# Kernel tuning notes

Hardware: AMD Instinct MI355X
Metric: run time of the kernel (lower is better)

The kernel has to match this reference:

```python
import jax, jax.numpy as jnp
import numpy as np

B, N, HW, PS, FHW = 16, 4096, 224, 8, 56

def _gelu(x):
    return jax.nn.gelu(x, approximate=True)  # tanh approximation, matches nn.GELU(approximate='tanh')

def _conv(x, w, b, stride):
    y = jax.lax.conv_general_dilated(x, w, (stride, stride), [(1, 1), (1, 1)],
                                     dimension_numbers=('NCHW', 'OIHW', 'NCHW'))
    return y + b[None, :, None, None]

def _embed(points):
    # for i in 0..11: append sin(2^i * p) then cos(2^i * p) -> [B,N,48]
    factors = 2.0 ** jnp.arange(12, dtype=points.dtype)
    scaled = points[..., None, :] * factors[:, None]          # [B,N,12,2]
    feats = jnp.concatenate([jnp.sin(scaled), jnp.cos(scaled)], axis=-1)  # [B,N,12,4]
    return feats.reshape(points.shape[0], points.shape[1], 48)

def _extract_patches(fmap, points):
    # fmap [B,C,H,W]; points in [0,1]; bilinear grid_sample, zeros padding, align_corners=True
    Bq, C, H, W = fmap.shape
    centers = points * 2.0 - 1.0
    step = 2.0 / (W - 1)
    half = (PS - 1) / 2.0
    offs = jnp.linspace(-half, half, PS, dtype=fmap.dtype) * step
    offx2d, offy2d = jnp.meshgrid(offs, offs, indexing='ij')   # [ps,ps]
    gx = centers[..., 0][..., None, None] + offx2d             # [B,N,ps,ps]
    gy = centers[..., 1][..., None, None] + offy2d
    # align_corners=True pixel coords
    ix = (gx + 1.0) * 0.5 * (W - 1)
    iy = (gy + 1.0) * 0.5 * (H - 1)
    x0f = jnp.floor(ix); y0f = jnp.floor(iy)
    x0 = x0f.astype(jnp.int32); y0 = y0f.astype(jnp.int32)
    x1 = x0 + 1; y1 = y0 + 1
    wx1 = ix - x0f; wx0 = 1.0 - wx1
    wy1 = iy - y0f; wy0 = 1.0 - wy1
    fflat = fmap.reshape(Bq, C, H * W)

    def corner(xi, yi, w):
        valid = ((xi >= 0) & (xi < W) & (yi >= 0) & (yi < H)).astype(fmap.dtype)
        idx = jnp.clip(yi, 0, H - 1) * W + jnp.clip(xi, 0, W - 1)   # [B,N,ps,ps]
        vals = jax.vmap(lambda f, i: f[:, i])(fflat, idx)           # [B,C,N,ps,ps]
        return vals * (w * valid)[:, None]

    out = (corner(x0, y0, wx0 * wy0) + corner(x1, y0, wx1 * wy0)
           + corner(x0, y1, wx0 * wy1) + corner(x1, y1, wx1 * wy1))  # [B,C,N,ps,ps]
    return out.transpose(0, 2, 1, 3, 4)                              # [B,N,C,ps,ps]

def setup_inputs():
    key = jax.random.key(0)
    ks = jax.random.split(key, 26)
    def w(k, shape):
        fan_in = int(np.prod(shape[1:]))
        return jax.random.normal(k, shape, jnp.float32) * (1.0 / np.sqrt(fan_in))
    inp = {
        'points': jax.random.uniform(ks[0], (B, N, 2), jnp.float32),
        'images': jax.random.normal(ks[1], (B, 3, HW, HW), jnp.float32),
        # plane encoder
        'pw1': w(ks[2], (16, 3, 3, 3)),  'pb1': jnp.zeros((16,), jnp.float32),
        'pw2': w(ks[3], (32, 16, 3, 3)), 'pb2': jnp.zeros((32,), jnp.float32),
        'pw3': w(ks[4], (4, 32, 3, 3)),  'pb3': jnp.zeros((4,), jnp.float32),
        # global encoder
        'gw1': w(ks[5], (4, 3, 3, 3)),   'gb1': jnp.zeros((4,), jnp.float32),
        'gw2': w(ks[6], (8, 4, 3, 3)),   'gb2': jnp.zeros((8,), jnp.float32),
        'gw3': w(ks[7], (16, 8, 3, 3)),  'gb3': jnp.zeros((16,), jnp.float32),
        'gw4': w(ks[8], (32, 16, 3, 3)), 'gb4': jnp.zeros((32,), jnp.float32),
        'gw5': w(ks[9], (64, 32, 3, 3)), 'gb5': jnp.zeros((64,), jnp.float32),
        # point encoder (torch Linear: [out,in])
        'lw1': w(ks[10], (256, 48)),  'lb1': jnp.zeros((256,), jnp.float32),
        'lw2': w(ks[11], (256, 256)), 'lb2': jnp.zeros((256,), jnp.float32),
        # head
        'hw1': w(ks[12], (512, 576)), 'hb1': jnp.zeros((512,), jnp.float32),
        'hw2': w(ks[13], (1, 512)),   'hb2': jnp.zeros((1,), jnp.float32),
    }
    return inp

def reference(points, images, pw1, pb1, pw2, pb2, pw3, pb3,
              gw1, gb1, gw2, gb2, gw3, gb3, gw4, gb4, gw5, gb5,
              lw1, lb1, lw2, lb2, hw1, hb1, hw2, hb2):
    # point branch
    pe = _embed(points)                                         # [B,N,48]
    pf = _gelu(pe @ lw1.T + lb1) @ lw2.T + lb2                  # [B,N,256]
    # plane encoder -> 4x56x56 fmap
    f = _gelu(_conv(images, pw1, pb1, 2))
    f = _gelu(_conv(f, pw2, pb2, 2))
    fmap = _gelu(_conv(f, pw3, pb3, 1))                         # [B,4,56,56]
    # global encoder -> [B,64]
    g = images
    for wg, bg in ((gw1, gb1), (gw2, gb2), (gw3, gb3), (gw4, gb4), (gw5, gb5)):
        g = _gelu(_conv(g, wg, bg, 2))
    gc = g.mean(axis=(2, 3))                                    # AvgPool2d(7)+Flatten -> [B,64]
    gc = jnp.broadcast_to(gc[:, None, :], (points.shape[0], points.shape[1], 64))
    # per-point bilinear patch gather
    patches = _extract_patches(fmap, points).reshape(points.shape[0], points.shape[1], -1)  # [B,N,256]
    fused = jnp.concatenate([pf, patches, gc], axis=-1)         # [B,N,576]
    logit = _gelu(fused @ hw1.T + hb1) @ hw2.T + hb2            # [B,N,1]
    return logit
```

## Files before the change

kernel.cpp:

```cpp
#include <hip/hip_runtime.h>
#include <math.h>

#define BB 16
#define NN 4096
#define M_TOT (BB*NN)
#define TBK 32

typedef __attribute__((ext_vector_type(8))) short s8v;
typedef __attribute__((ext_vector_type(4))) float f4v;

__device__ __forceinline__ float gelu_t(float x){
    float u = 1.5957691216057308f * x * (1.0f + 0.044715f*x*x);
    return x / (1.0f + __expf(-u));
}

__device__ __forceinline__ unsigned short f2bf(float f){
    unsigned int u = __float_as_uint(f);
    u += 0x7fffu + ((u >> 16) & 1u);
    return (unsigned short)(u >> 16);
}

#define GLL(src, dst) __builtin_amdgcn_global_load_lds( \
    (const __attribute__((address_space(1))) void*)(src), \
    (__attribute__((address_space(3))) void*)(dst), 16, 0, 0)

template<int CIN, int COUT, int STRIDE>
__global__ __launch_bounds__(256) void conv_tile_k(
    const float* __restrict__ in, const float* __restrict__ w,
    const float* __restrict__ bias, float* __restrict__ out,
    int Hin, int Win, int Hout, int Wout)
{
    constexpr int IW = 15*STRIDE + 3;
    constexpr int IH = IW;
    __shared__ float tile[IH][IW + 1];
    int tid = threadIdx.x;
    int tx = tid & 15, ty = tid >> 4;
    int b = blockIdx.z;
    int wo = blockIdx.x*16 + tx;
    int ho = blockIdx.y*16 + ty;
    int win0 = blockIdx.x*16*STRIDE - 1;
    int hin0 = blockIdx.y*16*STRIDE - 1;
    bool valid = (wo < Wout) && (ho < Hout);

    float acc[COUT];
    #pragma unroll
    for (int co = 0; co < COUT; ++co) acc[co] = bias[co];

    const float* ib = in + (size_t)(b*CIN)*Hin*Win;
    for (int ci = 0; ci < CIN; ++ci) {
        __syncthreads();
        const float* ic = ib + (size_t)ci*Hin*Win;
        for (int idx = tid; idx < IH*IW; idx += 256) {
            int r = idx / IW, c = idx - r*IW;
            int hi = hin0 + r, wi = win0 + c;
            float v = 0.f;
            if ((unsigned)hi < (unsigned)Hin && (unsigned)wi < (unsigned)Win)
                v = ic[hi*Win + wi];
            tile[r][c] = v;
        }
        __syncthreads();
        float vv[9];
        #pragma unroll
        for (int kh = 0; kh < 3; ++kh)
            #pragma unroll
            for (int kw = 0; kw < 3; ++kw)
                vv[kh*3+kw] = tile[ty*STRIDE + kh][tx*STRIDE + kw];
        const float* wc = w + ci*9;
        #pragma unroll
        for (int co = 0; co < COUT; ++co) {
            const float* wp = wc + co*CIN*9;
            #pragma unroll
            for (int k = 0; k < 9; ++k)
                acc[co] = fmaf(vv[k], wp[k], acc[co]);
        }
    }
    if (valid) {
        size_t obase = ((size_t)b*COUT)*Hout*Wout + (size_t)ho*Wout + wo;
        #pragma unroll
        for (int co = 0; co < COUT; ++co)
            out[obase + (size_t)co*Hout*Wout] = gelu_t(acc[co]);
    }
}

__global__ __launch_bounds__(256) void conv_p3_k(
    const float* __restrict__ in, const float* __restrict__ w,
    const float* __restrict__ bias, float4* __restrict__ out)
{
    __shared__ float tile[18][19];
    int tid = threadIdx.x;
    int tx = tid & 15, ty = tid >> 4;
    int b = blockIdx.z;
    int wo = blockIdx.x*16 + tx;
    int ho = blockIdx.y*16 + ty;
    int win0 = blockIdx.x*16 - 1;
    int hin0 = blockIdx.y*16 - 1;
    bool valid = (ho < 56) && (wo < 56);

    float acc[4];
    #pragma unroll
    for (int co = 0; co < 4; ++co) acc[co] = bias[co];

    const float* ib = in + (size_t)(b*32)*3136;
    for (int ci = 0; ci < 32; ++ci) {
        __syncthreads();
        const float* ic = ib + (size_t)ci*3136;
        for (int idx = tid; idx < 18*18; idx += 256) {
            int r = idx / 18, c = idx - r*18;
            int hi = hin0 + r, wi = win0 + c;
            float v = 0.f;
            if ((unsigned)hi < 56u && (unsigned)wi < 56u)
                v = ic[hi*56 + wi];
            tile[r][c] = v;
        }
        __syncthreads();
        float vv[9];
        #pragma unroll
        for (int kh = 0; kh < 3; ++kh)
            #pragma unroll
            for (int kw = 0; kw < 3; ++kw)
                vv[kh*3+kw] = tile[ty + kh][tx + kw];
        #pragma unroll
        for (int co = 0; co < 4; ++co) {
            const float* wp = w + co*288 + ci*9;
            #pragma unroll
            for (int k = 0; k < 9; ++k)
                acc[co] = fmaf(vv[k], wp[k], acc[co]);
        }
    }
    if (valid) {
        float4 o;
        o.x = gelu_t(acc[0]); o.y = gelu_t(acc[1]);
        o.z = gelu_t(acc[2]); o.w = gelu_t(acc[3]);
        out[(size_t)b*3136 + (size_t)ho*56 + wo] = o;
    }
}

__global__ __launch_bounds__(256) void conv_dual_k(
    const float* __restrict__ in,
    const float* __restrict__ wA, const float* __restrict__ bA,
    const float* __restrict__ wB, const float* __restrict__ bB,
    float* __restrict__ outA, float* __restrict__ outB)
{
    constexpr int IW = 33, IH = 33;
    const int Hin = 224, Win = 224, Hout = 112, Wout = 112;
    __shared__ float tile[IH][IW + 1];
    int tid = threadIdx.x;
    int tx = tid & 15, ty = tid >> 4;
    int b = blockIdx.z;
    int wo = blockIdx.x*16 + tx;
    int ho = blockIdx.y*16 + ty;
    int win0 = blockIdx.x*32 - 1;
    int hin0 = blockIdx.y*32 - 1;

    float accA[16], accB[4];
    #pragma unroll
    for (int co = 0; co < 16; ++co) accA[co] = bA[co];
    #pragma unroll
    for (int co = 0; co < 4; ++co) accB[co] = bB[co];

    const float* ib = in + (size_t)(b*3)*Hin*Win;
    for (int ci = 0; ci < 3; ++ci) {
        __syncthreads();
        const float* ic = ib + (size_t)ci*Hin*Win;
        for (int idx = tid; idx < IH*IW; idx += 256) {
            int r = idx / IW, c = idx - r*IW;
            int hi = hin0 + r, wi = win0 + c;
            float v = 0.f;
            if ((unsigned)hi < (unsigned)Hin && (unsigned)wi < (unsigned)Win)
                v = ic[hi*Win + wi];
            tile[r][c] = v;
        }
        __syncthreads();
        float vv[9];
        #pragma unroll
        for (int kh = 0; kh < 3; ++kh)
            #pragma unroll
            for (int kw = 0; kw < 3; ++kw)
                vv[kh*3+kw] = tile[ty*2 + kh][tx*2 + kw];
        #pragma unroll
        for (int co = 0; co < 16; ++co) {
            const float* wp = wA + co*27 + ci*9;
            #pragma unroll
            for (int k = 0; k < 9; ++k) accA[co] = fmaf(vv[k], wp[k], accA[co]);
        }
        #pragma unroll
        for (int co = 0; co < 4; ++co) {
            const float* wp = wB + co*27 + ci*9;
            #pragma unroll
            for (int k = 0; k < 9; ++k) accB[co] = fmaf(vv[k], wp[k], accB[co]);
        }
    }
    size_t px = (size_t)ho*Wout + wo;
    #pragma unroll
    for (int co = 0; co < 16; ++co)
        outA[((size_t)(b*16 + co))*Hout*Wout + px] = gelu_t(accA[co]);
    #pragma unroll
    for (int co = 0; co < 4; ++co)
        outB[((size_t)(b*4 + co))*Hout*Wout + px] = gelu_t(accB[co]);
}

__global__ void conv3x3_k(const float* __restrict__ in, const float* __restrict__ w,
                          const float* __restrict__ bias, float* __restrict__ out,
                          int Cin, int Hin, int Win, int Cout, int Hout, int Wout, int stride)
{
    int wo = blockIdx.x*blockDim.x + threadIdx.x;
    int ho = blockIdx.y*blockDim.y + threadIdx.y;
    int bc = blockIdx.z;
    int co = bc % Cout, b = bc / Cout;
    if (wo >= Wout || ho >= Hout) return;
    const float* wp = w + co*Cin*9;
    const float* ip = in + (size_t)(b*Cin)*Hin*Win;
    float acc = bias[co];
    int hbase = ho*stride - 1, wbase = wo*stride - 1;
    for (int ci = 0; ci < Cin; ++ci) {
        const float* ic = ip + (size_t)ci*Hin*Win;
        const float* wc = wp + ci*9;
        #pragma unroll
        for (int kh = 0; kh < 3; ++kh) {
            int hi = hbase + kh;
            if ((unsigned)hi >= (unsigned)Hin) continue;
            #pragma unroll
            for (int kw = 0; kw < 3; ++kw) {
                int wi = wbase + kw;
                if ((unsigned)wi >= (unsigned)Win) continue;
                acc = fmaf(ic[hi*Win + wi], wc[kh*3+kw], acc);
            }
        }
    }
    out[(((size_t)b*Cout + co)*Hout + ho)*Wout + wo] = gelu_t(acc);
}

__global__ void avgpool7_k(const float* __restrict__ in, float* __restrict__ out){
    int i = blockIdx.x*blockDim.x + threadIdx.x;
    if (i >= BB*64) return;
    const float* p = in + (size_t)i*49;
    float s = 0.f;
    #pragma unroll
    for (int k = 0; k < 49; ++k) s += p[k];
    out[i] = s * (1.0f/49.0f);
}

__global__ void cvtall_k(const float* __restrict__ lw1, const float* __restrict__ lw2,
                         const float* __restrict__ hw1, unsigned short* __restrict__ blw1,
                         unsigned short* __restrict__ blw2, unsigned short* __restrict__ bhw1){
    int i = blockIdx.x*blockDim.x + threadIdx.x;
    if (i < 256*64) {
        int r = i >> 6, c = i & 63;
        blw1[i] = (c < 48) ? f2bf(lw1[r*48 + c]) : 0;
        return;
    }
    i -= 256*64;
    if (i < 256*256) { blw2[i] = f2bf(lw2[i]); return; }
    i -= 256*256;
    if (i < 512*576) bhw1[i] = f2bf(hw1[i]);
}

__global__ __launch_bounds__(512) void mlp12_k(
    const float* __restrict__ points,
    const unsigned short* __restrict__ W1, const float* __restrict__ b1,
    const unsigned short* __restrict__ W2, const float* __restrict__ b2,
    unsigned short* __restrict__ C,
    const float4* __restrict__ fmap4, const float* __restrict__ gc)
{
    __shared__ unsigned short Hd[128*256];
    __shared__ unsigned short B2[256*TBK];
    int tid = threadIdx.x;
    int wv = tid >> 6, lane = tid & 63;
    int q = lane >> 4, lr = lane & 15;
    int mi = wv >> 2, ni = wv & 3;
    size_t m0 = (size_t)blockIdx.x * 128;

    f4v acc1[4][4];
    #pragma unroll
    for (int i = 0; i < 4; ++i)
        #pragma unroll
        for (int j = 0; j < 4; ++j) acc1[i][j] = (f4v){0.f,0.f,0.f,0.f};

    #pragma unroll
    for (int kb = 0; kb < 2; ++kb) {
        int seg = kb*4 + q;
        s8v a[4], b[4];
        #pragma unroll
        for (int t = 0; t < 4; ++t) {
            size_t m = m0 + mi*64 + t*16 + lr;
            float px = points[m*2], py = points[m*2+1];
            union { s8v v; unsigned short u[8]; } pk;
            #pragma unroll
            for (int j = 0; j < 8; ++j) {
                int k = seg*8 + j;
                unsigned short val = 0;
                if (k < 48) {
                    int i2 = k >> 2, rr = k & 3;
                    float f = (float)(1 << i2);
                    float p = (rr & 1) ? py : px;
                    float s = f * p;
                    val = f2bf((rr < 2) ? __sinf(s) : __cosf(s));
                }
                pk.u[j] = val;
            }
            a[t] = pk.v;
        }
        #pragma unroll
        for (int t = 0; t < 4; ++t) {
            int n = ni*64 + t*16 + lr;
            b[t] = *(const s8v*)(W1 + n*64 + seg*8);
        }
        #pragma unroll
        for (int mt = 0; mt < 4; ++mt)
            #pragma unroll
            for (int nt = 0; nt < 4; ++nt)
                acc1[mt][nt] = __builtin_amdgcn_mfma_f32_16x16x32_bf16(a[mt], b[nt], acc1[mt][nt], 0, 0, 0);
    }
    {
        float b1v[4];
        #pragma unroll
        for (int nt = 0; nt < 4; ++nt) b1v[nt] = b1[ni*64 + nt*16 + lr];
        #pragma unroll
        for (int mt = 0; mt < 4; ++mt)
            #pragma unroll
            for (int r4 = 0; r4 < 4; ++r4) {
                int row = mi*64 + mt*16 + q*4 + r4;
                #pragma unroll
                for (int nt = 0; nt < 4; ++nt) {
                    int col = ni*64 + nt*16 + lr;
                    float v = gelu_t(acc1[mt][nt][r4] + b1v[nt]);
                    int p = (col >> 3) ^ (row & 7);
                    Hd[(row*32 + p)*8 + (col & 7)] = f2bf(v);
                }
            }
    }
    __syncthreads();

    f4v acc2[4][4];
    #pragma unroll
    for (int i = 0; i < 4; ++i)
        #pragma unroll
        for (int j = 0; j < 4; ++j) acc2[i][j] = (f4v){0.f,0.f,0.f,0.f};

    for (int kt = 0; kt < 8; ++kt) {
        #pragma unroll
        for (int r = 0; r < 2; ++r) {
            int f = r*512 + tid;
            int rr = f >> 2, ll = (f & 3) ^ ((f >> 3) & 3);
            GLL(W2 + rr*256 + kt*32 + ll*8, B2 + f*8);
        }
        __syncthreads();
        s8v a[4], b[4];
        int sw = q ^ ((lr >> 1) & 3);
        #pragma unroll
        for (int t = 0; t < 4; ++t) {
            int row = mi*64 + t*16 + lr;
            int p = (kt*4 + q) ^ (row & 7);
            a[t] = *(const s8v*)(Hd + (row*32 + p)*8);
        }
        #pragma unroll
        for (int t = 0; t < 4; ++t) {
            int n = ni*64 + t*16 + lr;
            b[t] = *(const s8v*)(B2 + (n*4 + sw)*8);
        }
        #pragma unroll
        for (int mt = 0; mt < 4; ++mt)
            #pragma unroll
            for (int nt = 0; nt < 4; ++nt)
                acc2[mt][nt] = __builtin_amdgcn_mfma_f32_16x16x32_bf16(a[mt], b[nt], acc2[mt][nt], 0, 0, 0);
        __syncthreads();
    }
    {
        float b2v[4];
        #pragma unroll
        for (int nt = 0; nt < 4; ++nt) b2v[nt] = b2[ni*64 + nt*16 + lr];
        #pragma unroll
        for (int mt = 0; mt < 4; ++mt)
            #pragma unroll
            for (int r4 = 0; r4 < 4; ++r4) {
                size_t m = m0 + mi*64 + mt*16 + q*4 + r4;
                #pragma unroll
                for (int nt = 0; nt < 4; ++nt) {
                    int n = ni*64 + nt*16 + lr;
                    C[m*576 + n] = f2bf(acc2[mt][nt][r4] + b2v[nt]);
                }
            }
    }
    #pragma unroll 1
    for (int it = 0; it < 16; ++it) {
        int task = it*512 + tid;
        int ml = task >> 6, ij = task & 63;
        size_t m = m0 + ml;
        int i = ij >> 3, j = ij & 7;
        int b = (int)(m >> 12);
        float px = points[m*2], py = points[m*2+1];
        float cx = px*2.f - 1.f, cy = py*2.f - 1.f;
        const float step = 2.0f/55.0f;
        float gx = cx + ((float)i - 3.5f)*step;
        float gy = cy + ((float)j - 3.5f)*step;
        float ix = (gx + 1.f)*0.5f*55.f;
        float iy = (gy + 1.f)*0.5f*55.f;
        float x0f = floorf(ix), y0f = floorf(iy);
        int x0 = (int)x0f, y0 = (int)y0f;
        int x1 = x0 + 1,  y1 = y0 + 1;
        float wx1 = ix - x0f, wx0 = 1.f - wx1;
        float wy1 = iy - y0f, wy0 = 1.f - wy1;
        float v00 = ((x0>=0)&&(x0<56)&&(y0>=0)&&(y0<56)) ? 1.f : 0.f;
        float v10 = ((x1>=0)&&(x1<56)&&(y0>=0)&&(y0<56)) ? 1.f : 0.f;
        float v01 = ((x0>=0)&&(x0<56)&&(y1>=0)&&(y1<56)) ? 1.f : 0.f;
        float v11 = ((x1>=0)&&(x1<56)&&(y1>=0)&&(y1<56)) ? 1.f : 0.f;
        float w00 = wx0*wy0*v00, w10 = wx1*wy0*v10, w01 = wx0*wy1*v01, w11 = wx1*wy1*v11;
        int cx0 = min(max(x0,0),55), cx1 = min(max(x1,0),55);
        int cy0 = min(max(y0,0),55), cy1 = min(max(y1,0),55);
        const float4* fb = fmap4 + (size_t)b*3136;
        float4 f00 = fb[cy0*56 + cx0], f10 = fb[cy0*56 + cx1];
        float4 f01 = fb[cy1*56 + cx0], f11 = fb[cy1*56 + cx1];
        float4 v;
        v.x = w00*f00.x + w10*f10.x + w01*f01.x + w11*f11.x;
        v.y = w00*f00.y + w10*f10.y + w01*f01.y + w11*f11.y;
        v.z = w00*f00.z + w10*f10.z + w01*f01.z + w11*f11.z;
        v.w = w00*f00.w + w10*f10.w + w01*f01.w + w11*f11.w;
        C[m*576 + 256 +   0 + ij] = f2bf(v.x);
        C[m*576 + 256 +  64 + ij] = f2bf(v.y);
        C[m*576 + 256 + 128 + ij] = f2bf(v.z);
        C[m*576 + 256 + 192 + ij] = f2bf(v.w);
        C[m*576 + 512 + ij] = f2bf(gc[b*64 + ij]);
    }
}

__global__ __launch_bounds__(512) void gemm_hd_k(
    const unsigned short* __restrict__ A, int lda,
    const unsigned short* __restrict__ W, int ldw,
    const float* __restrict__ bias, const float* __restrict__ w2,
    const float* __restrict__ b2, float* __restrict__ out, int K)
{
    __shared__ unsigned short As[128*TBK];
    __shared__ unsigned short Bs[512*TBK];
    __shared__ float red[8*64];
    int tid = threadIdx.x;
    int wv = tid >> 6, lane = tid & 63;
    int q = lane >> 4, lr = lane & 15;
    int sw = q ^ ((lr >> 1) & 3);
    int ms = wv >> 2, nb = (wv & 3) * 128;
    const unsigned short* Ab = A + (size_t)blockIdx.x*128*lda;

    int rA = tid >> 2;
    int lA = (tid & 3) ^ ((rA >> 1) & 3);
    const unsigned short* srcA = Ab + (size_t)rA*lda + lA*8;
    unsigned short* dstA = As + tid*8;
    const unsigned short* srcB[4]; unsigned short* dstB[4];
    #pragma unroll
    for (int r = 0; r < 4; ++r) {
        int f = r*512 + tid;
        int rr = f >> 2, ll = (f & 3) ^ ((rr >> 1) & 3);
        srcB[r] = W + (size_t)rr*ldw + ll*8;
        dstB[r] = Bs + f*8;
    }

    f4v acc[4][8];
    #pragma unroll
    for (int i = 0; i < 4; ++i)
        #pragma unroll
        for (int j = 0; j < 8; ++j) acc[i][j] = (f4v){0.f,0.f,0.f,0.f};

    for (int k0 = 0; k0 < K; k0 += TBK) {
        GLL(srcA, dstA); srcA += TBK;
        #pragma unroll
        for (int r = 0; r < 4; ++r) { GLL(srcB[r], dstB[r]); srcB[r] += TBK; }
        __syncthreads();
        s8v a[4], b[8];
        #pragma unroll
        for (int t = 0; t < 4; ++t)
            a[t] = *(const s8v*)(As + (ms*64 + t*16 + lr)*TBK + sw*8);
        #pragma unroll
        for (int t = 0; t < 8; ++t)
            b[t] = *(const s8v*)(Bs + (nb + t*16 + lr)*TBK + sw*8);
        #pragma unroll
        for (int mt = 0; mt < 4; ++mt)
            #pragma unroll
            for (int nt = 0; nt < 8; ++nt)
                acc[mt][nt] = __builtin_amdgcn_mfma_f32_16x16x32_bf16(a[mt], b[nt], acc[mt][nt], 0, 0, 0);
        __syncthreads();
    }
    float bv[8], w2v[8];
    #pragma unroll
    for (int nt = 0; nt < 8; ++nt) {
        int n = nb + nt*16 + lr;
        bv[nt] = bias[n];
        w2v[nt] = w2[n];
    }
    #pragma unroll
    for (int mt = 0; mt < 4; ++mt)
        #pragma unroll
        for (int r4 = 0; r4 < 4; ++r4) {
            int ml = mt*16 + q*4 + r4;
            float s = 0.f;
            #pragma unroll
            for (int nt = 0; nt < 8; ++nt)
                s += gelu_t(acc[mt][nt][r4] + bv[nt]) * w2v[nt];
            #pragma unroll
            for (int off = 8; off > 0; off >>= 1) s += __shfl_down(s, off, 16);
            if (lr == 0) red[wv*64 + ml] = s;
        }
    __syncthreads();
    if (tid < 128) {
        int msf = tid >> 6, ml = tid & 63;
        float t = red[(msf*4+0)*64 + ml] + red[(msf*4+1)*64 + ml]
                + red[(msf*4+2)*64 + ml] + red[(msf*4+3)*64 + ml];
        out[blockIdx.x*128 + tid] = t + b2[0];
    }
}

extern "C" void kernel_launch(void* const* d_in, const int* in_sizes, int n_in,
                              void* d_out, int out_size, void* d_ws, size_t ws_size,
                              hipStream_t stream) {
    const float* points = (const float*)d_in[0];
    const float* images = (const float*)d_in[1];
    const float* pw1 = (const float*)d_in[2];  const float* pb1 = (const float*)d_in[3];
    const float* pw2 = (const float*)d_in[4];  const float* pb2 = (const float*)d_in[5];
    const float* pw3 = (const float*)d_in[6];  const float* pb3 = (const float*)d_in[7];
    const float* gw1 = (const float*)d_in[8];  const float* gb1 = (const float*)d_in[9];
    const float* gw2 = (const float*)d_in[10]; const float* gb2 = (const float*)d_in[11];
    const float* gw3 = (const float*)d_in[12]; const float* gb3 = (const float*)d_in[13];
    const float* gw4 = (const float*)d_in[14]; const float* gb4 = (const float*)d_in[15];
    const float* gw5 = (const float*)d_in[16]; const float* gb5 = (const float*)d_in[17];
    const float* lw1 = (const float*)d_in[18]; const float* lb1 = (const float*)d_in[19];
    const float* lw2 = (const float*)d_in[20]; const float* lb2 = (const float*)d_in[21];
    const float* hw1 = (const float*)d_in[22]; const float* hb1 = (const float*)d_in[23];
    const float* hw2 = (const float*)d_in[24]; const float* hb2 = (const float*)d_in[25];
    float* out = (float*)d_out;

    char* base = (char*)d_ws;
    unsigned short* fused_b = (unsigned short*)base;
    unsigned short* hid_b   = fused_b + (size_t)M_TOT*576;
    float4* fmap4 = (float4*)(hid_b + (size_t)M_TOT*256);
    float* gc   = (float*)(fmap4 + (size_t)16*3136);
    unsigned short* blw1 = (unsigned short*)(gc + 1024);
    unsigned short* blw2 = blw1 + 256*64;
    unsigned short* bhw1 = blw2 + 256*256;
    float* ct = (float*)base;
    float* f1 = ct;
    float* f2 = f1 + (size_t)16*16*112*112;
    float* g1 = f2 + (size_t)16*32*56*56;
    float* g2 = g1 + (size_t)16*4*112*112;
    float* g3 = g2 + (size_t)16*8*56*56;
    float* g4 = g3 + (size_t)16*16*28*28;
    float* g5 = g4 + (size_t)16*32*14*14;

    cvtall_k<<<1472, 256, 0, stream>>>(lw1, lw2, hw1, blw1, blw2, bhw1);
    conv_dual_k<<<dim3(7,7,16), 256, 0, stream>>>(images, pw1, pb1, gw1, gb1, f1, g1);
    conv_tile_k<16,32,2><<<dim3(4,4,16), 256, 0, stream>>>(f1, pw2, pb2, f2, 112,112, 56,56);
    conv_p3_k<<<dim3(4,4,16), 256, 0, stream>>>(f2, pw3, pb3, fmap4);
    conv_tile_k<4,8,2>  <<<dim3(4,4,16), 256, 0, stream>>>(g1, gw2, gb2, g2, 112,112, 56,56);
    conv_tile_k<8,16,2> <<<dim3(2,2,16), 256, 0, stream>>>(g2, gw3, gb3, g3,  56, 56, 28,28);
    conv3x3_k<<<dim3(2,2,16*32), dim3(8,8), 0, stream>>>(g3, gw4, gb4, g4, 16, 28, 28, 32, 14, 14, 2);
    conv3x3_k<<<dim3(1,1,16*64), dim3(8,8), 0, stream>>>(g4, gw5, gb5, g5, 32, 14, 14, 64,  7,  7, 2);
    avgpool7_k<<<4, 256, 0, stream>>>(g5, gc);
    mlp12_k<<<M_TOT/128, 512, 0, stream>>>(points, blw1, lb1, blw2, lb2, fused_b, fmap4, gc);
    gemm_hd_k<<<M_TOT/128, 512, 0, stream>>>(fused_b, 576, bhw1, 576, hb1, hw2, hb2, out, 576);
}
```

Before: 467.6 us.

## Merge encoder conv launches, fuse global tail convs+pool, load GEMM A directly

Pairs the plane and global encoder conv layers into shared launches (conv_pg2, conv_pg3) so independent small grids run concurrently, and replaces the last two global convs plus the average pool with one per-batch tail kernel working out of LDS. The head GEMM now reads the A operand straight from global memory into registers instead of staging it through LDS, and hardcodes K=576. The aim is to cut launch count, fill more of the GPU with the small conv grids, and shrink LDS traffic in the GEMM. The cost is uncoalesced per-lane A loads in the GEMM and a tail kernel that runs only 16 blocks with large LDS use.

```diff
diff --git a/kernel.cpp b/kernel.cpp
--- a/kernel.cpp
+++ b/kernel.cpp
@@ -25,21 +25,19 @@
     (__attribute__((address_space(3))) void*)(dst), 16, 0, 0)
 
 template<int CIN, int COUT, int STRIDE>
-__global__ __launch_bounds__(256) void conv_tile_k(
+__device__ __forceinline__ void conv_dev(
     const float* __restrict__ in, const float* __restrict__ w,
     const float* __restrict__ bias, float* __restrict__ out,
-    int Hin, int Win, int Hout, int Wout)
+    int Hin, int Win, int Hout, int Wout, int bx, int by, int b, float* tile)
 {
     constexpr int IW = 15*STRIDE + 3;
     constexpr int IH = IW;
-    __shared__ float tile[IH][IW + 1];
     int tid = threadIdx.x;
     int tx = tid & 15, ty = tid >> 4;
-    int b = blockIdx.z;
-    int wo = blockIdx.x*16 + tx;
-    int ho = blockIdx.y*16 + ty;
-    int win0 = blockIdx.x*16*STRIDE - 1;
-    int hin0 = blockIdx.y*16*STRIDE - 1;
+    int wo = bx*16 + tx;
+    int ho = by*16 + ty;
+    int win0 = bx*16*STRIDE - 1;
+    int hin0 = by*16*STRIDE - 1;
     bool valid = (wo < Wout) && (ho < Hout);
 
     float acc[COUT];
@@ -56,7 +54,7 @@
             float v = 0.f;
             if ((unsigned)hi < (unsigned)Hin && (unsigned)wi < (unsigned)Win)
                 v = ic[hi*Win + wi];
-            tile[r][c] = v;
+            tile[r*34 + c] = v;
         }
         __syncthreads();
         float vv[9];
@@ -64,7 +62,7 @@
         for (int kh = 0; kh < 3; ++kh)
             #pragma unroll
             for (int kw = 0; kw < 3; ++kw)
-                vv[kh*3+kw] = tile[ty*STRIDE + kh][tx*STRIDE + kw];
+                vv[kh*3+kw] = tile[(ty*STRIDE + kh)*34 + tx*STRIDE + kw];
         const float* wc = w + ci*9;
         #pragma unroll
         for (int co = 0; co < COUT; ++co) {
@@ -82,18 +80,17 @@
     }
 }
 
-__global__ __launch_bounds__(256) void conv_p3_k(
+__device__ __forceinline__ void conv_p3_dev(
     const float* __restrict__ in, const float* __restrict__ w,
-    const float* __restrict__ bias, float4* __restrict__ out)
-{
-    __shared__ float tile[18][19];
+    const float* __restrict__ bias, float4* __restrict__ out,
+    int bx, int by, int b, float* tile)
+{
     int tid = threadIdx.x;
     int tx = tid & 15, ty = tid >> 4;
-    int b = blockIdx.z;
-    int wo = blockIdx.x*16 + tx;
-    int ho = blockIdx.y*16 + ty;
-    int win0 = blockIdx.x*16 - 1;
-    int hin0 = blockIdx.y*16 - 1;
+    int wo = bx*16 + tx;
+    int ho = by*16 + ty;
+    int win0 = bx*16 - 1;
+    int hin0 = by*16 - 1;
     bool valid = (ho < 56) && (wo < 56);
 
     float acc[4];
@@ -110,7 +107,7 @@
             float v = 0.f;
             if ((unsigned)hi < 56u && (unsigned)wi < 56u)
                 v = ic[hi*56 + wi];
-            tile[r][c] = v;
+            tile[r*34 + c] = v;
         }
         __syncthreads();
         float vv[9];
@@ -118,7 +115,7 @@
         for (int kh = 0; kh < 3; ++kh)
             #pragma unroll
             for (int kw = 0; kw < 3; ++kw)
-                vv[kh*3+kw] = tile[ty + kh][tx + kw];
+                vv[kh*3+kw] = tile[(ty + kh)*34 + tx + kw];
         #pragma unroll
         for (int co = 0; co < 4; ++co) {
             const float* wp = w + co*288 + ci*9;
@@ -199,45 +196,100 @@
         outB[((size_t)(b*4 + co))*Hout*Wout + px] = gelu_t(accB[co]);
 }
 
-__global__ void conv3x3_k(const float* __restrict__ in, const float* __restrict__ w,
-                          const float* __restrict__ bias, float* __restrict__ out,
-                          int Cin, int Hin, int Win, int Cout, int Hout, int Wout, int stride)
-{
-    int wo = blockIdx.x*blockDim.x + threadIdx.x;
-    int ho = blockIdx.y*blockDim.y + threadIdx.y;
-    int bc = blockIdx.z;
-    int co = bc % Cout, b = bc / Cout;
-    if (wo >= Wout || ho >= Hout) return;
-    const float* wp = w + co*Cin*9;
-    const float* ip = in + (size_t)(b*Cin)*Hin*Win;
-    float acc = bias[co];
-    int hbase = ho*stride - 1, wbase = wo*stride - 1;
-    for (int ci = 0; ci < Cin; ++ci) {
-        const float* ic = ip + (size_t)ci*Hin*Win;
-        const float* wc = wp + ci*9;
-        #pragma unroll
-        for (int kh = 0; kh < 3; ++kh) {
-            int hi = hbase + kh;
-            if ((unsigned)hi >= (unsigned)Hin) continue;
-            #pragma unroll
-            for (int kw = 0; kw < 3; ++kw) {
-                int wi = wbase + kw;
-                if ((unsigned)wi >= (unsigned)Win) continue;
-                acc = fmaf(ic[hi*Win + wi], wc[kh*3+kw], acc);
+__global__ __launch_bounds__(256) void conv_pg2_k(
+    const float* __restrict__ f1, const float* __restrict__ pw2, const float* __restrict__ pb2, float* __restrict__ f2,
+    const float* __restrict__ g1, const float* __restrict__ gw2, const float* __restrict__ gb2, float* __restrict__ g2)
+{
+    __shared__ float tile[33*34];
+    int z = blockIdx.z;
+    if (z < 16) conv_dev<16,32,2>(f1, pw2, pb2, f2, 112,112, 56,56, blockIdx.x, blockIdx.y, z, tile);
+    else        conv_dev<4,8,2> (g1, gw2, gb2, g2, 112,112, 56,56, blockIdx.x, blockIdx.y, z-16, tile);
+}
+
+__global__ __launch_bounds__(256) void conv_pg3_k(
+    const float* __restrict__ f2, const float* __restrict__ pw3, const float* __restrict__ pb3, float4* __restrict__ fmap4,
+    const float* __restrict__ g2, const float* __restrict__ gw3, const float* __restrict__ gb3, float* __restrict__ g3)
+{
+    __shared__ float tile[33*34];
+    int z = blockIdx.z;
+    if (z < 16) {
+        conv_p3_dev(f2, pw3, pb3, fmap4, blockIdx.x, blockIdx.y, z, tile);
+    } else {
+        if (blockIdx.x >= 2 || blockIdx.y >= 2) return;
+        conv_dev<8,16,2>(g2, gw3, gb3, g3, 56,56, 28,28, blockIdx.x, blockIdx.y, z-16, tile);
+    }
+}
+
+__global__ __launch_bounds__(256) void tail_k(
+    const float* __restrict__ g3, const float* __restrict__ w4, const float* __restrict__ b4,
+    const float* __restrict__ w5, const float* __restrict__ b5, float* __restrict__ gc)
+{
+    __shared__ float s3[16*784];
+    __shared__ float s4[32*196];
+    __shared__ float s5[64*49];
+    int b = blockIdx.x, tid = threadIdx.x;
+    const float* src = g3 + (size_t)b*16*784;
+    for (int i = tid; i < 16*784; i += 256) s3[i] = src[i];
+    __syncthreads();
+    if (tid < 196) {
+        int ho = tid/14, wo = tid - (tid/14)*14;
+        float acc[32];
+        #pragma unroll
+        for (int co = 0; co < 32; ++co) acc[co] = b4[co];
+        for (int ci = 0; ci < 16; ++ci) {
+            #pragma unroll
+            for (int kh = 0; kh < 3; ++kh) {
+                int hi = ho*2 - 1 + kh;
+                if ((unsigned)hi >= 28u) continue;
+                #pragma unroll
+                for (int kw = 0; kw < 3; ++kw) {
+                    int wi = wo*2 - 1 + kw;
+                    if ((unsigned)wi >= 28u) continue;
+                    float v = s3[ci*784 + hi*28 + wi];
+                    int wofs = ci*9 + kh*3 + kw;
+                    #pragma unroll
+                    for (int co = 0; co < 32; ++co)
+                        acc[co] = fmaf(v, w4[co*144 + wofs], acc[co]);
+                }
             }
         }
-    }
-    out[(((size_t)b*Cout + co)*Hout + ho)*Wout + wo] = gelu_t(acc);
-}
-
-__global__ void avgpool7_k(const float* __restrict__ in, float* __restrict__ out){
-    int i = blockIdx.x*blockDim.x + threadIdx.x;
-    if (i >= BB*64) return;
-    const float* p = in + (size_t)i*49;
-    float s = 0.f;
-    #pragma unroll
-    for (int k = 0; k < 49; ++k) s += p[k];
-    out[i] = s * (1.0f/49.0f);
+        #pragma unroll
+        for (int co = 0; co < 32; ++co) s4[co*196 + tid] = gelu_t(acc[co]);
+    }
+    __syncthreads();
+    if (tid < 196) {
+        int px = tid % 49, cg = tid / 49;
+        int ho = px/7, wo = px - (px/7)*7;
+        float acc[16];
+        #pragma unroll
+        for (int c = 0; c < 16; ++c) acc[c] = b5[cg*16 + c];
+        for (int ci = 0; ci < 32; ++ci) {
+            #pragma unroll
+            for (int kh = 0; kh < 3; ++kh) {
+                int hi = ho*2 - 1 + kh;
+                if ((unsigned)hi >= 14u) continue;
+                #pragma unroll
+                for (int kw = 0; kw < 3; ++kw) {
+                    int wi = wo*2 - 1 + kw;
+                    if ((unsigned)wi >= 14u) continue;
+                    float v = s4[ci*196 + hi*14 + wi];
+                    int wofs = ci*9 + kh*3 + kw;
+                    #pragma unroll
+                    for (int c = 0; c < 16; ++c)
+                        acc[c] = fmaf(v, w5[(cg*16 + c)*288 + wofs], acc[c]);
+                }
+            }
+        }
+        #pragma unroll
+        for (int c = 0; c < 16; ++c) s5[(cg*16 + c)*49 + px] = gelu_t(acc[c]);
+    }
+    __syncthreads();
+    if (tid < 64) {
+        float s = 0.f;
+        #pragma unroll
+        for (int k = 0; k < 49; ++k) s += s5[tid*49 + k];
+        gc[b*64 + tid] = s * (1.0f/49.0f);
+    }
 }
 
 __global__ void cvtall_k(const float* __restrict__ lw1, const float* __restrict__ lw2,
@@ -424,12 +476,11 @@
 }
 
 __global__ __launch_bounds__(512) void gemm_hd_k(
-    const unsigned short* __restrict__ A, int lda,
-    const unsigned short* __restrict__ W, int ldw,
+    const unsigned short* __restrict__ A,
+    const unsigned short* __restrict__ W,
     const float* __restrict__ bias, const float* __restrict__ w2,
-    const float* __restrict__ b2, float* __restrict__ out, int K)
-{
-    __shared__ unsigned short As[128*TBK];
+    const float* __restrict__ b2, float* __restrict__ out)
+{
     __shared__ unsigned short Bs[512*TBK];
     __shared__ float red[8*64];
     int tid = threadIdx.x;
@@ -437,20 +488,20 @@
     int q = lane >> 4, lr = lane & 15;
     int sw = q ^ ((lr >> 1) & 3);
     int ms = wv >> 2, nb = (wv & 3) * 128;
-    const unsigned short* Ab = A + (size_t)blockIdx.x*128*lda;
-
-    int rA = tid >> 2;
-    int lA = (tid & 3) ^ ((rA >> 1) & 3);
-    const unsigned short* srcA = Ab + (size_t)rA*lda + lA*8;
-    unsigned short* dstA = As + tid*8;
+    size_t m0 = (size_t)blockIdx.x * 128;
+
     const unsigned short* srcB[4]; unsigned short* dstB[4];
     #pragma unroll
     for (int r = 0; r < 4; ++r) {
         int f = r*512 + tid;
         int rr = f >> 2, ll = (f & 3) ^ ((rr >> 1) & 3);
-        srcB[r] = W + (size_t)rr*ldw + ll*8;
+        srcB[r] = W + (size_t)rr*576 + ll*8;
         dstB[r] = Bs + f*8;
     }
+    const unsigned short* Arow[4];
+    #pragma unroll
+    for (int t = 0; t < 4; ++t)
+        Arow[t] = A + (m0 + ms*64 + t*16 + lr)*576 + q*8;
 
     f4v acc[4][8];
     #pragma unroll
@@ -458,15 +509,14 @@
         #pragma unroll
         for (int j = 0; j < 8; ++j) acc[i][j] = (f4v){0.f,0.f,0.f,0.f};
 
-    for (int k0 = 0; k0 < K; k0 += TBK) {
-        GLL(srcA, dstA); srcA += TBK;
+    for (int k0 = 0; k0 < 576; k0 += TBK) {
         #pragma unroll
         for (int r = 0; r < 4; ++r) { GLL(srcB[r], dstB[r]); srcB[r] += TBK; }
-        __syncthreads();
-        s8v a[4], b[8];
-        #pragma unroll
-        for (int t = 0; t < 4; ++t)
-            a[t] = *(const s8v*)(As + (ms*64 + t*16 + lr)*TBK + sw*8);
+        s8v a[4];
+        #pragma unroll
+        for (int t = 0; t < 4; ++t) { a[t] = *(const s8v*)(Arow[t]); Arow[t] += TBK; }
+        __syncthreads();
+        s8v b[8];
         #pragma unroll
         for (int t = 0; t < 8; ++t)
             b[t] = *(const s8v*)(Bs + (nb + t*16 + lr)*TBK + sw*8);
@@ -539,18 +589,12 @@
     float* g1 = f2 + (size_t)16*32*56*56;
     float* g2 = g1 + (size_t)16*4*112*112;
     float* g3 = g2 + (size_t)16*8*56*56;
-    float* g4 = g3 + (size_t)16*16*28*28;
-    float* g5 = g4 + (size_t)16*32*14*14;
 
     cvtall_k<<<1472, 256, 0, stream>>>(lw1, lw2, hw1, blw1, blw2, bhw1);
     conv_dual_k<<<dim3(7,7,16), 256, 0, stream>>>(images, pw1, pb1, gw1, gb1, f1, g1);
-    conv_tile_k<16,32,2><<<dim3(4,4,16), 256, 0, stream>>>(f1, pw2, pb2, f2, 112,112, 56,56);
-    conv_p3_k<<<dim3(4,4,16), 256, 0, stream>>>(f2, pw3, pb3, fmap4);
-    conv_tile_k<4,8,2>  <<<dim3(4,4,16), 256, 0, stream>>>(g1, gw2, gb2, g2, 112,112, 56,56);
-    conv_tile_k<8,16,2> <<<dim3(2,2,16), 256, 0, stream>>>(g2, gw3, gb3, g3,  56, 56, 28,28);
-    conv3x3_k<<<dim3(2,2,16*32), dim3(8,8), 0, stream>>>(g3, gw4, gb4, g4, 16, 28, 28, 32, 14, 14, 2);
-    conv3x3_k<<<dim3(1,1,16*64), dim3(8,8), 0, stream>>>(g4, gw5, gb5, g5, 32, 14, 14, 64,  7,  7, 2);
-    avgpool7_k<<<4, 256, 0, stream>>>(g5, gc);
+    conv_pg2_k<<<dim3(4,4,32), 256, 0, stream>>>(f1, pw2, pb2, f2, g1, gw2, gb2, g2);
+    conv_pg3_k<<<dim3(4,4,32), 256, 0, stream>>>(f2, pw3, pb3, fmap4, g2, gw3, gb3, g3);
+    tail_k<<<16, 256, 0, stream>>>(g3, gw4, gb4, gw5, gb5, gc);
     mlp12_k<<<M_TOT/128, 512, 0, stream>>>(points, blw1, lb1, blw2, lb2, fused_b, fmap4, gc);
-    gemm_hd_k<<<M_TOT/128, 512, 0, stream>>>(fused_b, 576, bhw1, 576, hb1, hw2, hb2, out, 576);
-}
+    gemm_hd_k<<<M_TOT/128, 512, 0, stream>>>(fused_b, bhw1, hb1, hw2, hb2, out);
+}
```

New measurement: 468.5 us. Within noise of the previous version (+0.2%).
